# Kernel tuning notes

Measured on AMD Instinct MI355X. Metric: run time of the kernel, lower is better.

Reference implementation:

```python
import jax, jax.numpy as jnp
import numpy as np

B, D = 4, 128          # batch, spatial grid size
N = 160000
CIN, COUT, K = 32, 32, 27
EPS = 1e-5             # torch BatchNorm1d default
SLOPE = 0.01           # torch LeakyReLU default


def _build_sparse_topology():
    """Random unique active voxel coords + 27-neighbor indice pairs (-1 = missing)."""
    rng = np.random.default_rng(0)
    total = B * D * D * D
    lin = np.sort(rng.choice(total, size=N, replace=False)).astype(np.int64)
    b = lin // (D * D * D)
    rem = lin % (D * D * D)
    z, y, x = rem // (D * D), (rem // D) % D, rem % D
    lut = np.full(total, -1, np.int32)
    lut[lin] = np.arange(N, dtype=np.int32)
    nbr = np.full((N, K), -1, np.int32)
    k = 0
    for dz in (-1, 0, 1):
        for dy in (-1, 0, 1):
            for dx in (-1, 0, 1):
                zz, yy, xx = z + dz, y + dy, x + dx
                valid = (zz >= 0) & (zz < D) & (yy >= 0) & (yy < D) & (xx >= 0) & (xx < D)
                nl = ((b * D + zz) * D + yy) * D + xx
                nbr[valid, k] = lut[nl[valid]]
                k += 1
    return nbr


def setup_inputs() -> dict:
    key = jax.random.key(0)
    kf, kw, kb = jax.random.split(key, 3)
    neighbor_idx = jnp.asarray(_build_sparse_topology())
    features = jax.random.normal(kf, (N, CIN), dtype=jnp.float32)
    w_scale = 1.0 / np.sqrt(K * CIN)
    weight = jax.random.normal(kw, (K, CIN, COUT), dtype=jnp.float32) * w_scale
    bias = jax.random.normal(kb, (COUT,), dtype=jnp.float32) * 0.01
    gamma = jnp.ones((COUT,), dtype=jnp.float32)
    beta = jnp.zeros((COUT,), dtype=jnp.float32)
    return {"features": features, "neighbor_idx": neighbor_idx, "weight": weight,
            "bias": bias, "gamma": gamma, "beta": beta}


def reference(features, neighbor_idx, weight, bias, gamma, beta):
    # --- submanifold 3x3x3 sparse conv: gather -> per-offset GEMM -> accumulate ---
    mask = (neighbor_idx >= 0)                       # [N,27]
    idx = jnp.maximum(neighbor_idx, 0)
    gathered = features[idx] * mask[..., None].astype(features.dtype)  # [N,27,Cin]
    out = jnp.einsum('nkc,kcd->nd', gathered, weight) + bias           # [N,Cout]
    # --- BatchNorm1d (training-mode batch stats, biased variance) ---
    mean = jnp.mean(out, axis=0)
    var = jnp.var(out, axis=0)
    out = (out - mean) * jax.lax.rsqrt(var + EPS) * gamma + beta
    # --- LeakyReLU ---
    return jnp.where(out >= 0, out, SLOPE * out)
```

## Files before the change

kernel.cpp:

```cpp
#include <hip/hip_runtime.h>

#define NVOX  160000
#define KOFF  27
#define EPSV  1e-5f
#define SLOPE 0.01f
#define NBLK  2500
#define PADP  2560

using bf16x8 = __attribute__((ext_vector_type(8))) __bf16;
using f32x4  = __attribute__((ext_vector_type(4))) float;
using i32x4  = __attribute__((ext_vector_type(4))) int;
using u16    = unsigned short;
typedef __attribute__((ext_vector_type(4), aligned(4))) int i32x4u;
typedef __attribute__((ext_vector_type(2), aligned(4))) int i32x2u;


__global__ void pack_weights(const float* __restrict__ w, u16* __restrict__ wp) {
    int tid = blockIdx.x * blockDim.x + threadIdx.x;
    if (tid >= KOFF * 2 * 64 * 8) return;
    int j = tid & 7;
    int L = (tid >> 3) & 63;
    int f = (tid >> 9) & 1;
    int k = tid >> 10;
    int c = ((L >> 4) << 3) + j;
    int d = (f << 4) + (L & 15);
    __bf16 b = (__bf16)w[(k * 32 + c) * 32 + d];
    wp[tid] = __builtin_bit_cast(u16, b);
}

__global__ __launch_bounds__(256) void conv_f32(
    const float* __restrict__ feat,
    const int*  __restrict__ nbr,
    const i32x4* __restrict__ wp,
    float* __restrict__ out,
    float* __restrict__ partials)
{
    const int lane  = threadIdx.x & 63;
    const int wid   = (blockIdx.x * 256 + threadIdx.x) >> 6;
    const int vbase = wid * 16;
    const int m = lane & 15;
    const int q = lane >> 4;

    const int* row = nbr + (size_t)(vbase + m) * KOFF;
    int id[27];
    *(i32x4u*)(id +  0) = *(const i32x4u*)(row +  0);
    *(i32x4u*)(id +  4) = *(const i32x4u*)(row +  4);
    *(i32x4u*)(id +  8) = *(const i32x4u*)(row +  8);
    *(i32x4u*)(id + 12) = *(const i32x4u*)(row + 12);
    *(i32x4u*)(id + 16) = *(const i32x4u*)(row + 16);
    *(i32x4u*)(id + 20) = *(const i32x4u*)(row + 20);
    *(i32x2u*)(id + 24) = *(const i32x2u*)(row + 24);
    id[26] = row[26];

    f32x4 acc0 = {}, acc1 = {};

#pragma unroll
    for (int b = 0; b < 3; ++b) {
        f32x4 lo[9], hi[9];
#pragma unroll
        for (int j = 0; j < 9; ++j) {
            int k = b * 9 + j;
            if (__ballot(id[k] >= 0)) {
                int v_id = id[k];
                int safe = v_id >= 0 ? v_id : 0;
                const f32x4* fp = (const f32x4*)(feat + (size_t)safe * 32 + q * 8);
                lo[j] = fp[0];
                hi[j] = fp[1];
            }
        }
#pragma unroll
        for (int j = 0; j < 9; ++j) {
            int k = b * 9 + j;
            if (__ballot(id[k] >= 0)) {
                bf16x8 t;
#pragma unroll
                for (int jj = 0; jj < 4; ++jj) {
                    t[jj]     = (__bf16)lo[j][jj];
                    t[4 + jj] = (__bf16)hi[j][jj];
                }
                bf16x8 z = {};
                bf16x8 a = (id[k] < 0) ? z : t;
                i32x4 b0r = wp[(k * 2 + 0) * 64 + lane];
                i32x4 b1r = wp[(k * 2 + 1) * 64 + lane];
                bf16x8 b0 = __builtin_bit_cast(bf16x8, b0r);
                bf16x8 b1 = __builtin_bit_cast(bf16x8, b1r);
                acc0 = __builtin_amdgcn_mfma_f32_16x16x32_bf16(a, b0, acc0, 0, 0, 0);
                acc1 = __builtin_amdgcn_mfma_f32_16x16x32_bf16(a, b1, acc1, 0, 0, 0);
            }
        }
    }

    float s0 = 0, s1 = 0, sq0 = 0, sq1 = 0;
#pragma unroll
    for (int r = 0; r < 4; ++r) {
        int v = vbase + q * 4 + r;
        float x0 = acc0[r], x1 = acc1[r];
        s0 += x0; sq0 += x0 * x0;
        s1 += x1; sq1 += x1 * x1;
        out[v * 32 + m]      = x0;
        out[v * 32 + 16 + m] = x1;
    }
    s0  += __shfl_xor(s0, 16, 64);  s0  += __shfl_xor(s0, 32, 64);
    s1  += __shfl_xor(s1, 16, 64);  s1  += __shfl_xor(s1, 32, 64);
    sq0 += __shfl_xor(sq0, 16, 64); sq0 += __shfl_xor(sq0, 32, 64);
    sq1 += __shfl_xor(sq1, 16, 64); sq1 += __shfl_xor(sq1, 32, 64);

    __shared__ float red[4][64];
    int w = threadIdx.x >> 6;
    if (lane < 16) {
        red[w][m]      = s0;
        red[w][16 + m] = s1;
        red[w][32 + m] = sq0;
        red[w][48 + m] = sq1;
    }
    __syncthreads();
    if (threadIdx.x < 64) {
        int t = threadIdx.x;
        partials[(size_t)t * PADP + blockIdx.x] =
            red[0][t] + red[1][t] + red[2][t] + red[3][t];
    }
}

__global__ __launch_bounds__(256) void reduce_stats(
    const float* __restrict__ partials, float* __restrict__ stats)
{
    const float* prow = partials + (size_t)blockIdx.x * PADP;
    float s = 0.f;
    for (int p = threadIdx.x; p < NBLK; p += 256) s += prow[p];
#pragma unroll
    for (int off = 1; off < 64; off <<= 1) s += __shfl_xor(s, off, 64);
    __shared__ float sd[4];
    int lane = threadIdx.x & 63, w = threadIdx.x >> 6;
    if (lane == 0) sd[w] = s;
    __syncthreads();
    if (threadIdx.x == 0) stats[blockIdx.x] = sd[0] + sd[1] + sd[2] + sd[3];
}

__global__ __launch_bounds__(256) void apply_bn(
    f32x4* __restrict__ o, const float* __restrict__ stats,
    const float* __restrict__ gamma, const float* __restrict__ beta)
{
    __shared__ float s[64];
    int t = threadIdx.x;
    if (t < 32) {
        float mean = stats[t] * (1.f / NVOX);
        float var  = stats[32 + t] * (1.f / NVOX) - mean * mean;
        float rstd = rsqrtf(var + EPSV);
        float scale = gamma[t] * rstd;
        s[t]      = scale;
        s[32 + t] = beta[t] - mean * scale;
    }
    __syncthreads();
    int i = blockIdx.x * 256 + t;
#pragma unroll
    for (int rep = 0; rep < 2; ++rep) {
        int i2 = i * 2 + rep;
        f32x4 v = o[i2];
        int c0 = (i2 & 7) * 4;
        f32x4 r;
#pragma unroll
        for (int j = 0; j < 4; ++j) {
            float y = v[j] * s[c0 + j] + s[32 + c0 + j];
            r[j] = (y >= 0.f) ? y : SLOPE * y;
        }
        o[i2] = r;
    }
}

extern "C" void kernel_launch(void* const* d_in, const int* in_sizes, int n_in,
                              void* d_out, int out_size, void* d_ws, size_t ws_size,
                              hipStream_t stream) {
    const float* feat  = (const float*)d_in[0];
    const int*   nbr   = (const int*)d_in[1];
    const float* w     = (const float*)d_in[2];
    const float* gamma = (const float*)d_in[4];
    const float* beta  = (const float*)d_in[5];

    char* ws = (char*)d_ws;
    float* partials = (float*)ws;
    u16*   wp       = (u16*)(ws + 655360);
    float* stats    = (float*)(ws + 655360 + 55296);

    pack_weights<<<108, 256, 0, stream>>>(w, wp);
    conv_f32<<<NBLK, 256, 0, stream>>>(feat, nbr, (const i32x4*)wp,
                                       (float*)d_out, partials);
    reduce_stats<<<64, 256, 0, stream>>>(partials, stats);
    apply_bn<<<2500, 256, 0, stream>>>((f32x4*)d_out, stats, gamma, beta);
}
```

Before: 124.4 us.

## Replace partials buffer and reduce kernel with padded atomics; stage neighbor rows in LDS

The per-block partial-sum buffer and the separate reduce_stats kernel are removed. Each conv block now atomically adds its 64 channel sums into a stats array padded to one value per 16 floats, and pack_weights zeroes that array first. Neighbor index rows are now loaded cooperatively into shared memory with coalesced loads, replacing the per-lane unaligned vector loads from global memory. This drops one kernel launch and a global round trip, at the cost of 2500-way atomic contention per channel, non-deterministic summation order, and an extra barrier plus LDS traffic.

```diff
diff --git a/kernel.cpp b/kernel.cpp
--- a/kernel.cpp
+++ b/kernel.cpp
@@ -5,18 +5,21 @@
 #define EPSV  1e-5f
 #define SLOPE 0.01f
 #define NBLK  2500
-#define PADP  2560
+#define SPAD  16
 
 using bf16x8 = __attribute__((ext_vector_type(8))) __bf16;
 using f32x4  = __attribute__((ext_vector_type(4))) float;
 using i32x4  = __attribute__((ext_vector_type(4))) int;
 using u16    = unsigned short;
-typedef __attribute__((ext_vector_type(4), aligned(4))) int i32x4u;
-typedef __attribute__((ext_vector_type(2), aligned(4))) int i32x2u;
 
 
-__global__ void pack_weights(const float* __restrict__ w, u16* __restrict__ wp) {
+__global__ void pack_weights(const float* __restrict__ w, u16* __restrict__ wp,
+                             float* __restrict__ stats) {
     int tid = blockIdx.x * blockDim.x + threadIdx.x;
+    if (blockIdx.x == 0) {
+        int t = threadIdx.x;
+        stats[t] = 0.f; stats[256 + t] = 0.f; stats[512 + t] = 0.f; stats[768 + t] = 0.f;
+    }
     if (tid >= KOFF * 2 * 64 * 8) return;
     int j = tid & 7;
     int L = (tid >> 3) & 63;
@@ -33,7 +36,7 @@
     const int*  __restrict__ nbr,
     const i32x4* __restrict__ wp,
     float* __restrict__ out,
-    float* __restrict__ partials)
+    float* __restrict__ stats)
 {
     const int lane  = threadIdx.x & 63;
     const int wid   = (blockIdx.x * 256 + threadIdx.x) >> 6;
@@ -41,27 +44,33 @@
     const int m = lane & 15;
     const int q = lane >> 4;
 
-    const int* row = nbr + (size_t)(vbase + m) * KOFF;
-    int id[27];
-    *(i32x4u*)(id +  0) = *(const i32x4u*)(row +  0);
-    *(i32x4u*)(id +  4) = *(const i32x4u*)(row +  4);
-    *(i32x4u*)(id +  8) = *(const i32x4u*)(row +  8);
-    *(i32x4u*)(id + 12) = *(const i32x4u*)(row + 12);
-    *(i32x4u*)(id + 16) = *(const i32x4u*)(row + 16);
-    *(i32x4u*)(id + 20) = *(const i32x4u*)(row + 20);
-    *(i32x2u*)(id + 24) = *(const i32x2u*)(row + 24);
-    id[26] = row[26];
+    __shared__ int   nlds[64 * KOFF];
+    __shared__ float red[4][64];
+
+    {
+        const int* src = nbr + (size_t)(blockIdx.x * 64) * KOFF;
+#pragma unroll
+        for (int i = 0; i < 7; ++i) {
+            int idx = threadIdx.x + i * 256;
+            if (idx < 64 * KOFF) nlds[idx] = src[idx];
+        }
+    }
+    __syncthreads();
+
+    const int* myrow = nlds + ((threadIdx.x >> 6) * 16 + m) * KOFF;
 
     f32x4 acc0 = {}, acc1 = {};
 
 #pragma unroll
     for (int b = 0; b < 3; ++b) {
         f32x4 lo[9], hi[9];
+        int   idb[9];
 #pragma unroll
         for (int j = 0; j < 9; ++j) {
             int k = b * 9 + j;
-            if (__ballot(id[k] >= 0)) {
-                int v_id = id[k];
+            idb[j] = myrow[k];
+            if (__ballot(idb[j] >= 0)) {
+                int v_id = idb[j];
                 int safe = v_id >= 0 ? v_id : 0;
                 const f32x4* fp = (const f32x4*)(feat + (size_t)safe * 32 + q * 8);
                 lo[j] = fp[0];
@@ -71,7 +80,7 @@
 #pragma unroll
         for (int j = 0; j < 9; ++j) {
             int k = b * 9 + j;
-            if (__ballot(id[k] >= 0)) {
+            if (__ballot(idb[j] >= 0)) {
                 bf16x8 t;
 #pragma unroll
                 for (int jj = 0; jj < 4; ++jj) {
@@ -79,7 +88,7 @@
                     t[4 + jj] = (__bf16)hi[j][jj];
                 }
                 bf16x8 z = {};
-                bf16x8 a = (id[k] < 0) ? z : t;
+                bf16x8 a = (idb[j] < 0) ? z : t;
                 i32x4 b0r = wp[(k * 2 + 0) * 64 + lane];
                 i32x4 b1r = wp[(k * 2 + 1) * 64 + lane];
                 bf16x8 b0 = __builtin_bit_cast(bf16x8, b0r);
@@ -105,7 +114,6 @@
     sq0 += __shfl_xor(sq0, 16, 64); sq0 += __shfl_xor(sq0, 32, 64);
     sq1 += __shfl_xor(sq1, 16, 64); sq1 += __shfl_xor(sq1, 32, 64);
 
-    __shared__ float red[4][64];
     int w = threadIdx.x >> 6;
     if (lane < 16) {
         red[w][m]      = s0;
@@ -116,24 +124,9 @@
     __syncthreads();
     if (threadIdx.x < 64) {
         int t = threadIdx.x;
-        partials[(size_t)t * PADP + blockIdx.x] =
-            red[0][t] + red[1][t] + red[2][t] + red[3][t];
+        float v = red[0][t] + red[1][t] + red[2][t] + red[3][t];
+        atomicAdd(&stats[(size_t)t * SPAD], v);
     }
-}
-
-__global__ __launch_bounds__(256) void reduce_stats(
-    const float* __restrict__ partials, float* __restrict__ stats)
-{
-    const float* prow = partials + (size_t)blockIdx.x * PADP;
-    float s = 0.f;
-    for (int p = threadIdx.x; p < NBLK; p += 256) s += prow[p];
-#pragma unroll
-    for (int off = 1; off < 64; off <<= 1) s += __shfl_xor(s, off, 64);
-    __shared__ float sd[4];
-    int lane = threadIdx.x & 63, w = threadIdx.x >> 6;
-    if (lane == 0) sd[w] = s;
-    __syncthreads();
-    if (threadIdx.x == 0) stats[blockIdx.x] = sd[0] + sd[1] + sd[2] + sd[3];
 }
 
 __global__ __launch_bounds__(256) void apply_bn(
@@ -143,8 +136,8 @@
     __shared__ float s[64];
     int t = threadIdx.x;
     if (t < 32) {
-        float mean = stats[t] * (1.f / NVOX);
-        float var  = stats[32 + t] * (1.f / NVOX) - mean * mean;
+        float mean = stats[(size_t)t * SPAD] * (1.f / NVOX);
+        float var  = stats[(size_t)(32 + t) * SPAD] * (1.f / NVOX) - mean * mean;
         float rstd = rsqrtf(var + EPSV);
         float scale = gamma[t] * rstd;
         s[t]      = scale;
@@ -177,13 +170,11 @@
     const float* beta  = (const float*)d_in[5];
 
     char* ws = (char*)d_ws;
-    float* partials = (float*)ws;
-    u16*   wp       = (u16*)(ws + 655360);
-    float* stats    = (float*)(ws + 655360 + 55296);
+    u16*   wp    = (u16*)ws;
+    float* stats = (float*)(ws + 57344);
 
-    pack_weights<<<108, 256, 0, stream>>>(w, wp);
+    pack_weights<<<108, 256, 0, stream>>>(w, wp, stats);
     conv_f32<<<NBLK, 256, 0, stream>>>(feat, nbr, (const i32x4*)wp,
-                                       (float*)d_out, partials);
-    reduce_stats<<<64, 256, 0, stream>>>(partials, stats);
+                                       (float*)d_out, stats);
     apply_bn<<<2500, 256, 0, stream>>>((f32x4*)d_out, stats, gamma, beta);
 }
```

Measured after the change: 161.2 us. 1.3x slower.
